# Kernel optimization log

Hardware: AMD Instinct MI355X
Metric: run time of the kernel (lower is better)

## Reference

```python
import jax, jax.numpy as jnp
import numpy as np

B, C, H, W = 8, 512, 64, 64
G = 32  # GroupNorm groups
EPS = 1e-5


def setup_inputs() -> dict:
    key = jax.random.key(0)
    ks = jax.random.split(key, 5)
    x = jax.random.normal(ks[0], (B, C, H, W), dtype=jnp.float32)
    gn_w = jnp.ones((C,), jnp.float32)
    gn_b = jnp.zeros((C,), jnp.float32)
    # 1x1 convs == channel-mixing matmuls; kaiming-ish init scale
    qkv_w = jax.random.normal(ks[1], (3 * C, C), jnp.float32) / np.sqrt(C)
    qkv_b = jnp.zeros((3 * C,), jnp.float32)
    proj_w = jax.random.normal(ks[2], (C, C), jnp.float32) / np.sqrt(C)
    proj_b = jnp.zeros((C,), jnp.float32)
    return {"x": x, "gn_w": gn_w, "gn_b": gn_b, "qkv_w": qkv_w,
            "qkv_b": qkv_b, "proj_w": proj_w, "proj_b": proj_b}


def _group_norm(x, w, b):
    Bv, Cv, Hv, Wv = x.shape
    xr = x.reshape(Bv, G, Cv // G, Hv * Wv)
    mu = xr.mean(axis=(2, 3), keepdims=True)
    var = xr.var(axis=(2, 3), keepdims=True)
    xn = ((xr - mu) * jax.lax.rsqrt(var + EPS)).reshape(Bv, Cv, Hv, Wv)
    return xn * w[None, :, None, None] + b[None, :, None, None]


def reference(x, gn_w, gn_b, qkv_w, qkv_b, proj_w, proj_b):
    Bv, Cv, Hv, Wv = x.shape
    T = Hv * Wv
    h = _group_norm(x, gn_w, gn_b)
    # 1x1 conv -> [B, 3C, T]
    qkv = jnp.einsum('bchw,oc->bohw', h, qkv_w) + qkv_b[None, :, None, None]
    qkv = qkv.reshape(Bv, 3, Cv, T)
    q, k, v = qkv[:, 0], qkv[:, 1], qkv[:, 2]  # each [B, C, T]
    scale = Cv ** -0.25  # 1/sqrt(sqrt(C)), applied to q and k
    attn = jnp.einsum('bct,bcs->bts', q * scale, k * scale)  # [B, T, T]
    attn = jax.nn.softmax(attn, axis=-1)
    out = jnp.einsum('bts,bcs->bct', attn, v).reshape(Bv, Cv, Hv, Wv)
    out = jnp.einsum('bchw,oc->bohw', out, proj_w) + proj_b[None, :, None, None]
    return x + out
```

## Files before the change

### kernel.cpp

```cpp
#include <hip/hip_runtime.h>

typedef unsigned short u16;
typedef unsigned int   u32;
typedef unsigned long long u64;

typedef __attribute__((ext_vector_type(8)))  short short8;
typedef __attribute__((ext_vector_type(4)))  short short4v;
typedef __attribute__((ext_vector_type(4)))  float float4v;
typedef __attribute__((ext_vector_type(16))) float float16v;

#define NB 8
#define NC 512
#define NT 4096
#define NO 1536
#define SCALE_QK 0.04419417382415922f
#define LOG2E_   1.4426950408889634f

__device__ inline u16 f2b(float f){
  u32 u = __builtin_bit_cast(u32, f);
  u += 0x7fffu + ((u >> 16) & 1u);
  return (u16)(u >> 16);
}

typedef __attribute__((address_space(1))) const unsigned int as1c_uint;
typedef __attribute__((address_space(3))) unsigned int as3_uint;

__device__ inline void gload16(const void* g, void* l){
  __builtin_amdgcn_global_load_lds((as1c_uint*)g, (as3_uint*)l, 16, 0, 0);
}

__device__ inline short8 ld8pair(const u16* p){
  short4v a = *(const short4v*)(p);
  short4v b = *(const short4v*)(p + 4);
  return __builtin_shufflevector(a, b, 0,1,2,3,4,5,6,7);
}

__global__ void k_cvt(const float* __restrict__ src, u16* __restrict__ dst, int n){
  int i = blockIdx.x*256 + threadIdx.x;
  if (i < n) dst[i] = f2b(src[i]);
}

__global__ void k_stats(const float* __restrict__ x, float* __restrict__ stats){
  int bg = blockIdx.x;
  int tid = threadIdx.x;
  const float4* p = (const float4*)(x + (size_t)bg*65536);
  float s = 0.f, q = 0.f;
  for (int i=0;i<64;i++){
    float4 v = p[i*256 + tid];
    s += v.x+v.y+v.z+v.w;
    q += v.x*v.x + v.y*v.y + v.z*v.z + v.w*v.w;
  }
  __shared__ float ls[256], lq[256];
  ls[tid]=s; lq[tid]=q; __syncthreads();
  for (int off=128; off>0; off>>=1){
    if (tid < off){ ls[tid]+=ls[tid+off]; lq[tid]+=lq[tid+off]; }
    __syncthreads();
  }
  if (tid==0){
    float mean = ls[0]*(1.f/65536.f);
    float var  = lq[0]*(1.f/65536.f) - mean*mean;
    stats[bg*2]   = mean;
    stats[bg*2+1] = rsqrtf(var + 1e-5f);
  }
}

__global__ void k_gn_apply(const float* __restrict__ x, const float* __restrict__ stats,
                           const float* __restrict__ gw, const float* __restrict__ gb,
                           u16* __restrict__ h){
  __shared__ u16 lt[64*65];
  int b = blockIdx.z, c0 = blockIdx.y*64, t0 = blockIdx.x*64;
  int tid = threadIdx.x;
  for (int it=0; it<16; it++){
    int idx = it*256 + tid;
    int cl = idx>>6, tl = idx&63;
    int c = c0 + cl;
    float v = x[((size_t)b*NC + c)*NT + t0 + tl];
    float mean = stats[(b*32 + (c>>4))*2];
    float rstd = stats[(b*32 + (c>>4))*2 + 1];
    float y = (v - mean)*rstd*gw[c] + gb[c];
    lt[cl*65 + tl] = f2b(y);
  }
  __syncthreads();
  for (int it=0; it<16; it++){
    int idx = it*256 + tid;
    int tw = idx>>6, cw = idx&63;
    h[((size_t)b*NT + t0 + tw)*NC + c0 + cw] = lt[cw*65 + tw];
  }
}

__device__ inline void stage128(const u16* gbase, u16* lbuf, int w, int l){
  #pragma unroll
  for (int i=0;i<4;i++){
    int r0 = (w*4+i)*8;
    int lr = r0 + (l>>3);
    int gch = (l&7) ^ (lr&7);
    gload16(gbase + (size_t)lr*512 + gch*8, lbuf + r0*64);
  }
}

__device__ inline void tile_mac(const u16* sA, const u16* sB, float4v acc[4][4], int wm, int wn, int l){
  #pragma unroll
  for (int kk=0; kk<2; kk++){
    short8 af[4], bf[4];
    #pragma unroll
    for (int f=0; f<4; f++){
      int rowA = wm + f*16 + (l&15);
      int chA  = (kk*4 + (l>>4)) ^ (rowA&7);
      af[f] = *(const short8*)(sA + rowA*64 + chA*8);
      int rowB = wn + f*16 + (l&15);
      int chB  = (kk*4 + (l>>4)) ^ (rowB&7);
      bf[f] = *(const short8*)(sB + rowB*64 + chB*8);
    }
    #pragma unroll
    for (int fm=0; fm<4; fm++)
      #pragma unroll
      for (int fn=0; fn<4; fn++)
        acc[fm][fn] = __builtin_amdgcn_mfma_f32_16x16x32_bf16(af[fm], bf[fn], acc[fm][fn], 0,0,0);
  }
}

__global__ __launch_bounds__(256,2) void k_qkv_gemm(const u16* __restrict__ h, const u16* __restrict__ wq,
                                                    const float* __restrict__ qb, u16* __restrict__ qkv,
                                                    u16* __restrict__ vct){
  __shared__ __align__(16) u16 lA[2][8192];
  __shared__ __align__(16) u16 lB[2][8192];
  int b = blockIdx.z, t0 = blockIdx.y*128, o0 = blockIdx.x*128;
  int tid = threadIdx.x, w = tid>>6, l = tid&63;
  int wm = (w&1)*64, wn = (w>>1)*64;
  float4v acc[4][4];
  #pragma unroll
  for (int i=0;i<4;i++)
    #pragma unroll
    for (int j=0;j<4;j++)
      #pragma unroll
      for (int e=0;e<4;e++) acc[i][j][e] = 0.f;
  const u16* Ab = h  + ((size_t)b*NT + t0)*NC;
  const u16* Bb = wq + (size_t)o0*NC;
  stage128(Ab, lA[0], w, l);
  stage128(Bb, lB[0], w, l);
  __syncthreads();
  for (int it=0; it<8; it++){
    int cur = it&1;
    if (it < 7){
      stage128(Ab + (it+1)*64, lA[cur^1], w, l);
      stage128(Bb + (it+1)*64, lB[cur^1], w, l);
    }
    tile_mac(lA[cur], lB[cur], acc, wm, wn, l);
    __syncthreads();
  }
  u16* ep = ((w < 2) ? (u16*)lA : (u16*)lB) + (w&1)*4352;
  if (o0 < 1024){
    #pragma unroll
    for (int fn=0; fn<4; fn++){
      float bs = qb[o0 + wn + fn*16 + (l&15)];
      #pragma unroll
      for (int fm=0; fm<4; fm++)
        #pragma unroll
        for (int r=0; r<4; r++){
          int tl_ = fm*16 + (l>>4)*4 + r;
          int ol_ = fn*16 + (l&15);
          ep[tl_*68 + ol_] = f2b(acc[fm][fn][r] + bs);
        }
    }
    __syncthreads();
    #pragma unroll
    for (int i=0;i<8;i++){
      int r  = i*8 + (l>>3);
      int c8 = (l&7)*8;
      short8 v8 = ld8pair(ep + r*68 + c8);
      *(short8*)(qkv + ((size_t)b*NT + t0 + wm + r)*NO + o0 + wn + c8) = v8;
    }
  } else {
    #pragma unroll
    for (int fn=0; fn<4; fn++){
      float bs = qb[o0 + wn + fn*16 + (l&15)];
      #pragma unroll
      for (int fm=0; fm<4; fm++)
        #pragma unroll
        for (int r=0; r<4; r++){
          int ol_ = fn*16 + (l&15);
          int tl_ = fm*16 + (l>>4)*4 + r;
          ep[ol_*68 + tl_] = f2b(acc[fm][fn][r] + bs);
        }
    }
    __syncthreads();
    u16* vrow = vct + ((size_t)b*NC + (o0-1024) + wn + l)*NT + t0 + wm;
    #pragma unroll
    for (int i=0;i<8;i++){
      short8 v8 = ld8pair(ep + l*68 + i*8);
      *(short8*)(vrow + i*8) = v8;
    }
  }
}

__global__ __launch_bounds__(512,2) void k_attn(const u16* __restrict__ qkv, const u16* __restrict__ vct,
                                                u16* __restrict__ at){
  __shared__ __align__(16) u16 lK[2][16384];
  __shared__ __align__(16) u16 lV[2][16384];
  __shared__ __align__(16) u16 lP[128*36];
  __shared__ float lAl[128];
  __shared__ float lLs[128];
  __shared__ int   lFlag[8];
  const int bid = blockIdx.x;
  const int b = bid & 7;
  const int t0 = (bid >> 3) * 128;
  const int tid = threadIdx.x, w = tid>>6, l = tid&63;
  const int l15 = l&15, l4 = l>>4, l31 = l&31, l5 = l>>5;
  const int pm = w>>1, pc = w&1;
  const u16* qkv_b = qkv + (size_t)b*NT*NO;
  const u16* vct_b = vct + (size_t)b*NC*NT;

  short8 qf[16];
  {
    const u16* qrow = qkv_b + (size_t)(t0 + w*16 + l15)*NO;
    #pragma unroll
    for (int ks=0; ks<16; ks++) qf[ks] = *(const short8*)(qrow + ks*32 + l4*8);
  }
  float16v acc[8];
  #pragma unroll
  for (int i=0;i<8;i++)
    #pragma unroll
    for (int j=0;j<16;j++) acc[i][j] = 0.f;
  float M_r[4] = {-1e30f,-1e30f,-1e30f,-1e30f};
  float L_r[4] = {0.f,0.f,0.f,0.f};

  #pragma unroll
  for (int i=0;i<4;i++){
    int sl = w*4+i;
    gload16(qkv_b + (size_t)sl*NO + 512 + (l ^ (sl&7))*8, &lK[0][sl*512]);
  }
  #pragma unroll
  for (int i=0;i<4;i++){
    int g = w*4+i, chunk = g>>3, c0 = (g&7)*64;
    gload16(vct_b + (size_t)(c0 + l)*NT + chunk*8, &lV[0][chunk*4096 + c0*8]);
  }
  __syncthreads();

  int cur = 0;
  for (int st=0; st<128; st++){
    if (st < 127){
      const int s1 = st*32 + 32;
      #pragma unroll
      for (int i=0;i<4;i++){
        int sl = w*4+i;
        gload16(qkv_b + (size_t)(s1+sl)*NO + 512 + (l ^ (sl&7))*8, &lK[cur^1][sl*512]);
      }
      #pragma unroll
      for (int i=0;i<4;i++){
        int g = w*4+i, chunk = g>>3, c0 = (g&7)*64;
        gload16(vct_b + (size_t)(c0 + l)*NT + s1 + chunk*8, &lV[cur^1][chunk*4096 + c0*8]);
      }
    }

    float4v Lf0, Lf1;
    #pragma unroll
    for (int e=0;e<4;e++){ Lf0[e]=0.f; Lf1[e]=0.f; }
    #pragma unroll
    for (int ks=0; ks<16; ks++){
      int gch = ks*4 + l4;
      int sA = l15;
      short8 b0 = *(const short8*)(&lK[cur][sA*512 + ((gch ^ (sA&7))*8)]);
      int sB = 16 + l15;
      short8 b1 = *(const short8*)(&lK[cur][sB*512 + ((gch ^ (sB&7))*8)]);
      Lf0 = __builtin_amdgcn_mfma_f32_16x16x32_bf16(qf[ks], b0, Lf0, 0,0,0);
      Lf1 = __builtin_amdgcn_mfma_f32_16x16x32_bf16(qf[ks], b1, Lf1, 0,0,0);
    }

    float v0[4], v1[4], mxA[4];
    bool need = false;
    #pragma unroll
    for (int r=0; r<4; r++){
      v0[r] = Lf0[r]*SCALE_QK; v1[r] = Lf1[r]*SCALE_QK;
      float mx = fmaxf(v0[r], v1[r]);
      mx = fmaxf(mx, __shfl_xor(mx,1));
      mx = fmaxf(mx, __shfl_xor(mx,2));
      mx = fmaxf(mx, __shfl_xor(mx,4));
      mx = fmaxf(mx, __shfl_xor(mx,8));
      mxA[r] = mx;
      need = need || (mx > M_r[r] + 4.0f);
    }
    int nw = __any((int)need);
    #pragma unroll
    for (int r=0; r<4; r++){
      float mnew = nw ? fmaxf(M_r[r], mxA[r]) : M_r[r];
      float al   = nw ? exp2f((M_r[r] - mnew)*LOG2E_) : 1.0f;
      float p0 = exp2f((v0[r] - mnew)*LOG2E_);
      float p1 = exp2f((v1[r] - mnew)*LOG2E_);
      L_r[r] = L_r[r]*al + (p0 + p1);
      M_r[r] = mnew;
      int tl_ = w*16 + l4*4 + r;
      lP[tl_*36 + l15]      = f2b(p0);
      lP[tl_*36 + 16 + l15] = f2b(p1);
      if (l15 == 0) lAl[tl_] = al;
    }
    if (l == 0) lFlag[w] = nw;

    asm volatile("s_waitcnt lgkmcnt(0)" ::: "memory");
    __builtin_amdgcn_sched_barrier(0);
    __builtin_amdgcn_s_barrier();
    __builtin_amdgcn_sched_barrier(0);

    {
      int doresc = lFlag[2*pm] | lFlag[2*pm+1];
      if (doresc){
        float4v a_[4];
        #pragma unroll
        for (int q=0;q<4;q++) a_[q] = *(const float4v*)(&lAl[pm*32 + q*8 + l5*4]);
        #pragma unroll
        for (int fn=0; fn<8; fn++)
          #pragma unroll
          for (int q=0;q<4;q++)
            #pragma unroll
            for (int rr=0;rr<4;rr++) acc[fn][q*4+rr] *= a_[q][rr];
      }
      const u16* prow = &lP[(pm*32 + l31)*36];
      short8 pa0 = ld8pair(prow + l5*8);
      short8 pa1 = ld8pair(prow + 16 + l5*8);
      const u16* vbase = &lV[cur][(pc*256 + l31)*8];
      __builtin_amdgcn_s_setprio(1);
      #pragma unroll
      for (int fn=0; fn<8; fn++){
        short8 vb0 = *(const short8*)(vbase + l5*4096 + fn*256);
        short8 vb1 = *(const short8*)(vbase + (2+l5)*4096 + fn*256);
        acc[fn] = __builtin_amdgcn_mfma_f32_32x32x16_bf16(pa0, vb0, acc[fn], 0,0,0);
        acc[fn] = __builtin_amdgcn_mfma_f32_32x32x16_bf16(pa1, vb1, acc[fn], 0,0,0);
      }
      __builtin_amdgcn_s_setprio(0);
    }
    __syncthreads();
    cur ^= 1;
  }

  #pragma unroll
  for (int r=0; r<4; r++){
    float s = L_r[r];
    s += __shfl_xor(s,1); s += __shfl_xor(s,2);
    s += __shfl_xor(s,4); s += __shfl_xor(s,8);
    if (l15 == 0) lLs[w*16 + l4*4 + r] = s;
  }
  __syncthreads();
  {
    float4v iv[4];
    #pragma unroll
    for (int q=0;q<4;q++){
      float4v t_ = *(const float4v*)(&lLs[pm*32 + q*8 + l5*4]);
      #pragma unroll
      for (int rr=0;rr<4;rr++) iv[q][rr] = 1.f/t_[rr];
    }
    #pragma unroll
    for (int fn=0; fn<8; fn++){
      int cc = pc*256 + fn*32 + l31;
      #pragma unroll
      for (int q=0;q<4;q++)
        #pragma unroll
        for (int rr=0;rr<4;rr++){
          int tt = t0 + pm*32 + rr + q*8 + l5*4;
          at[((size_t)b*NT + tt)*NC + cc] = f2b(acc[fn][q*4+rr]*iv[q][rr]);
        }
    }
  }
}

__global__ __launch_bounds__(256,2) void k_proj_res(const u16* __restrict__ wp, const u16* __restrict__ at,
                                                    const float* __restrict__ pb, const float* __restrict__ x,
                                                    float* __restrict__ out){
  __shared__ __align__(16) u16 lA[2][8192];
  __shared__ __align__(16) u16 lB[2][8192];
  int b = blockIdx.z, t0 = blockIdx.x*128, o0 = blockIdx.y*128;
  int tid = threadIdx.x, w = tid>>6, l = tid&63;
  int wm = (w&1)*64, wn = (w>>1)*64;
  float4v acc[4][4];
  #pragma unroll
  for (int i=0;i<4;i++)
    #pragma unroll
    for (int j=0;j<4;j++)
      #pragma unroll
      for (int e=0;e<4;e++) acc[i][j][e] = 0.f;
  const u16* Ab = wp + (size_t)o0*NC;
  const u16* Bb = at + ((size_t)b*NT + t0)*NC;
  stage128(Ab, lA[0], w, l);
  stage128(Bb, lB[0], w, l);
  __syncthreads();
  for (int it=0; it<8; it++){
    int cur = it&1;
    if (it < 7){
      stage128(Ab + (it+1)*64, lA[cur^1], w, l);
      stage128(Bb + (it+1)*64, lB[cur^1], w, l);
    }
    tile_mac(lA[cur], lB[cur], acc, wm, wn, l);
    __syncthreads();
  }
  #pragma unroll
  for (int fm=0; fm<4; fm++)
    #pragma unroll
    for (int r=0; r<4; r++){
      int o = o0 + wm + fm*16 + (l>>4)*4 + r;
      float bs = pb[o];
      #pragma unroll
      for (int fn=0; fn<4; fn++){
        int t = t0 + wn + fn*16 + (l&15);
        size_t idx = ((size_t)b*NC + o)*NT + t;
        out[idx] = acc[fm][fn][r] + bs + x[idx];
      }
    }
}

extern "C" void kernel_launch(void* const* d_in, const int* in_sizes, int n_in,
                              void* d_out, int out_size, void* d_ws, size_t ws_size,
                              hipStream_t stream){
  const float* x    = (const float*)d_in[0];
  const float* gnw  = (const float*)d_in[1];
  const float* gnb  = (const float*)d_in[2];
  const float* qkvw = (const float*)d_in[3];
  const float* qkvb = (const float*)d_in[4];
  const float* pw   = (const float*)d_in[5];
  const float* pb   = (const float*)d_in[6];
  float* out = (float*)d_out;

  char* ws = (char*)d_ws;
  float* stats = (float*)ws;
  u16* h   = (u16*)(ws + 4096);
  u16* qkv = (u16*)(ws + 4096 + 33554432);
  u16* vct = (u16*)(ws + 4096 + 33554432 + 100663296);
  u16* wqb = (u16*)(ws + 4096 + 33554432 + 100663296 + 33554432);
  u16* wpb = (u16*)(ws + 4096 + 33554432 + 100663296 + 33554432 + 1572864);
  u16* at  = h;

  k_cvt<<<3072, 256, 0, stream>>>(qkvw, wqb, 786432);
  k_cvt<<<1024, 256, 0, stream>>>(pw, wpb, 262144);
  k_stats<<<256, 256, 0, stream>>>(x, stats);
  k_gn_apply<<<dim3(64,8,8), 256, 0, stream>>>(x, stats, gnw, gnb, h);
  k_qkv_gemm<<<dim3(12,32,8), 256, 0, stream>>>(h, wqb, qkvb, qkv, vct);
  k_attn<<<256, 512, 0, stream>>>(qkv, vct, at);
  k_proj_res<<<dim3(32,4,8), 256, 0, stream>>>(wpb, at, pb, x, out);
}
```

Measured before the change: 1.079 ms.

## Make each warp own its 16 query rows for PV to drop mid-step barrier

The PV product is re-partitioned so each wave computes output for the same 16 query rows it produced scores for, across all 512 channels. It uses 16x16x32 MFMAs over 32 channel tiles instead of sharing P across wave pairs with 32x32 MFMAs. This removes the block-wide barrier between softmax and PV, the shared alpha/flag/row-sum arrays, and the cross-wave rescale lookup. In exchange each wave reads the full V tile from LDS, so V LDS traffic rises roughly fourfold, and smaller MFMAs may lower matrix throughput.

```diff
diff --git a/kernel.cpp b/kernel.cpp
--- a/kernel.cpp
+++ b/kernel.cpp
@@ -7,7 +7,6 @@
 typedef __attribute__((ext_vector_type(8)))  short short8;
 typedef __attribute__((ext_vector_type(4)))  short short4v;
 typedef __attribute__((ext_vector_type(4)))  float float4v;
-typedef __attribute__((ext_vector_type(16))) float float16v;
 
 #define NB 8
 #define NC 512
@@ -197,18 +196,15 @@
                                                 u16* __restrict__ at){
   __shared__ __align__(16) u16 lK[2][16384];
   __shared__ __align__(16) u16 lV[2][16384];
-  __shared__ __align__(16) u16 lP[128*36];
-  __shared__ float lAl[128];
-  __shared__ float lLs[128];
-  __shared__ int   lFlag[8];
+  __shared__ __align__(16) u16 lP[8*16*40];
   const int bid = blockIdx.x;
   const int b = bid & 7;
   const int t0 = (bid >> 3) * 128;
   const int tid = threadIdx.x, w = tid>>6, l = tid&63;
-  const int l15 = l&15, l4 = l>>4, l31 = l&31, l5 = l>>5;
-  const int pm = w>>1, pc = w&1;
+  const int l15 = l&15, l4 = l>>4;
   const u16* qkv_b = qkv + (size_t)b*NT*NO;
   const u16* vct_b = vct + (size_t)b*NC*NT;
+  u16* lPw = lP + w*640;
 
   short8 qf[16];
   {
@@ -216,11 +212,11 @@
     #pragma unroll
     for (int ks=0; ks<16; ks++) qf[ks] = *(const short8*)(qrow + ks*32 + l4*8);
   }
-  float16v acc[8];
-  #pragma unroll
-  for (int i=0;i<8;i++)
-    #pragma unroll
-    for (int j=0;j<16;j++) acc[i][j] = 0.f;
+  float4v acc[32];
+  #pragma unroll
+  for (int i=0;i<32;i++)
+    #pragma unroll
+    for (int e=0;e<4;e++) acc[i][e] = 0.f;
   float M_r[4] = {-1e30f,-1e30f,-1e30f,-1e30f};
   float L_r[4] = {0.f,0.f,0.f,0.f};
 
@@ -280,50 +276,34 @@
       need = need || (mx > M_r[r] + 4.0f);
     }
     int nw = __any((int)need);
+    float al[4];
     #pragma unroll
     for (int r=0; r<4; r++){
       float mnew = nw ? fmaxf(M_r[r], mxA[r]) : M_r[r];
-      float al   = nw ? exp2f((M_r[r] - mnew)*LOG2E_) : 1.0f;
+      al[r] = nw ? exp2f((M_r[r] - mnew)*LOG2E_) : 1.0f;
       float p0 = exp2f((v0[r] - mnew)*LOG2E_);
       float p1 = exp2f((v1[r] - mnew)*LOG2E_);
-      L_r[r] = L_r[r]*al + (p0 + p1);
+      L_r[r] = L_r[r]*al[r] + (p0 + p1);
       M_r[r] = mnew;
-      int tl_ = w*16 + l4*4 + r;
-      lP[tl_*36 + l15]      = f2b(p0);
-      lP[tl_*36 + 16 + l15] = f2b(p1);
-      if (l15 == 0) lAl[tl_] = al;
-    }
-    if (l == 0) lFlag[w] = nw;
-
-    asm volatile("s_waitcnt lgkmcnt(0)" ::: "memory");
-    __builtin_amdgcn_sched_barrier(0);
-    __builtin_amdgcn_s_barrier();
-    __builtin_amdgcn_sched_barrier(0);
+      int tl_ = l4*4 + r;
+      lPw[tl_*40 + l15]      = f2b(p0);
+      lPw[tl_*40 + 16 + l15] = f2b(p1);
+    }
 
     {
-      int doresc = lFlag[2*pm] | lFlag[2*pm+1];
-      if (doresc){
-        float4v a_[4];
+      if (nw){
         #pragma unroll
-        for (int q=0;q<4;q++) a_[q] = *(const float4v*)(&lAl[pm*32 + q*8 + l5*4]);
-        #pragma unroll
-        for (int fn=0; fn<8; fn++)
+        for (int ct=0; ct<32; ct++)
           #pragma unroll
-          for (int q=0;q<4;q++)
-            #pragma unroll
-            for (int rr=0;rr<4;rr++) acc[fn][q*4+rr] *= a_[q][rr];
+          for (int r=0; r<4; r++) acc[ct][r] *= al[r];
       }
-      const u16* prow = &lP[(pm*32 + l31)*36];
-      short8 pa0 = ld8pair(prow + l5*8);
-      short8 pa1 = ld8pair(prow + 16 + l5*8);
-      const u16* vbase = &lV[cur][(pc*256 + l31)*8];
+      short8 paf = *(const short8*)(lPw + l15*40 + l4*8);
+      const u16* vbase = &lV[cur][l4*4096 + l15*8];
       __builtin_amdgcn_s_setprio(1);
       #pragma unroll
-      for (int fn=0; fn<8; fn++){
-        short8 vb0 = *(const short8*)(vbase + l5*4096 + fn*256);
-        short8 vb1 = *(const short8*)(vbase + (2+l5)*4096 + fn*256);
-        acc[fn] = __builtin_amdgcn_mfma_f32_32x32x16_bf16(pa0, vb0, acc[fn], 0,0,0);
-        acc[fn] = __builtin_amdgcn_mfma_f32_32x32x16_bf16(pa1, vb1, acc[fn], 0,0,0);
+      for (int ct=0; ct<32; ct++){
+        short8 vbf = *(const short8*)(vbase + ct*128);
+        acc[ct] = __builtin_amdgcn_mfma_f32_16x16x32_bf16(paf, vbf, acc[ct], 0,0,0);
       }
       __builtin_amdgcn_s_setprio(0);
     }
@@ -331,32 +311,21 @@
     cur ^= 1;
   }
 
+  float iv[4];
   #pragma unroll
   for (int r=0; r<4; r++){
     float s = L_r[r];
     s += __shfl_xor(s,1); s += __shfl_xor(s,2);
     s += __shfl_xor(s,4); s += __shfl_xor(s,8);
-    if (l15 == 0) lLs[w*16 + l4*4 + r] = s;
-  }
-  __syncthreads();
-  {
-    float4v iv[4];
-    #pragma unroll
-    for (int q=0;q<4;q++){
-      float4v t_ = *(const float4v*)(&lLs[pm*32 + q*8 + l5*4]);
-      #pragma unroll
-      for (int rr=0;rr<4;rr++) iv[q][rr] = 1.f/t_[rr];
-    }
-    #pragma unroll
-    for (int fn=0; fn<8; fn++){
-      int cc = pc*256 + fn*32 + l31;
-      #pragma unroll
-      for (int q=0;q<4;q++)
-        #pragma unroll
-        for (int rr=0;rr<4;rr++){
-          int tt = t0 + pm*32 + rr + q*8 + l5*4;
-          at[((size_t)b*NT + tt)*NC + cc] = f2b(acc[fn][q*4+rr]*iv[q][rr]);
-        }
+    iv[r] = 1.f/s;
+  }
+  #pragma unroll
+  for (int ct=0; ct<32; ct++){
+    int cc = ct*16 + l15;
+    #pragma unroll
+    for (int r=0; r<4; r++){
+      int tt = t0 + w*16 + l4*4 + r;
+      at[((size_t)b*NT + tt)*NC + cc] = f2b(acc[ct][r]*iv[r]);
     }
   }
 }
```

New measurement: 966.6 us. 1.12x faster.
